# Kernel tuning notes

Measured on AMD Instinct MI355X. Metric: run time of the kernel, lower is better.

The kernel has to match this reference:

```python
import jax, jax.numpy as jnp
import numpy as np


def setup_inputs() -> dict:
    key = jax.random.key(0)
    kq, kk, kv, km = jax.random.split(key, 4)
    B, H, S, D = 2, 16, 2048, 64
    q = jax.random.normal(kq, (B, H, S, D), dtype=jnp.float32)
    k = jax.random.normal(kk, (B, H, S, D), dtype=jnp.float32)
    v = jax.random.normal(kv, (B, H, S, D), dtype=jnp.float32)
    mask = jax.random.randint(km, (B, 1, S, S), 0, 2, dtype=jnp.int32)
    return {"q": q, "k": k, "v": v, "mask": mask}


def reference(q, k, v, mask):
    # Scaled dot-product attention: softmax(Q K^T / sqrt(D)) V
    D = q.shape[-1]
    scale = jnp.asarray(1.0 / np.sqrt(D), q.dtype)
    score = jnp.einsum("bhqd,bhkd->bhqk", q, k) * scale  # [B,H,S,S]
    score = jnp.where(mask == 0, jnp.asarray(-10000.0, score.dtype), score)
    attn = jax.nn.softmax(score, axis=-1)
    out = jnp.einsum("bhqk,bhkd->bhqd", attn, v)  # [B,H,S,D]
    return (out, attn)
```

## Files before the change

### kernel.cpp

```cpp
#include <hip/hip_runtime.h>
#include <stdint.h>

typedef __attribute__((ext_vector_type(8))) short short8;
typedef __attribute__((ext_vector_type(4))) float f32x4;

#define B_ 2
#define H_ 16
#define S_ 2048
#define D_ 64
#define KB_ 64
#define NT_ (S_ / KB_)

__device__ __forceinline__ unsigned pk2(float x, float y) {
  const unsigned a = __builtin_bit_cast(unsigned, x) + 0x8000u;
  const unsigned b = __builtin_bit_cast(unsigned, y) + 0x8000u;
  return (a >> 16) | (b & 0xffff0000u);
}
__device__ __forceinline__ short b16(float x) {
  return (short)((__builtin_bit_cast(unsigned, x) + 0x8000u) >> 16);
}

__device__ __forceinline__ void block_barrier() {
  __asm__ volatile("s_waitcnt lgkmcnt(0)\n\ts_barrier" ::: "memory");
}
__device__ __forceinline__ void lgkm0() {
  __asm__ volatile("s_waitcnt lgkmcnt(0)" ::: "memory");
}

__global__ __launch_bounds__(256, 4)
void attn_kernel(const float* __restrict__ Q, const float* __restrict__ K,
                 const float* __restrict__ V, const int* __restrict__ M,
                 float* __restrict__ O, float* __restrict__ A)
{
  const int bid = blockIdx.x + (blockIdx.y << 5);
  const int qt  = (bid >> 3) & 31;
  const int bh  = (bid & 7) | ((bid >> 8) << 3);
  const int b   = bh >> 4;

  const int tid  = threadIdx.x;
  const int wave = tid >> 6;
  const int lane = tid & 63;
  const int l15  = lane & 15;
  const int quad = lane >> 4;

  const float* Qp = Q + (size_t)bh * S_ * D_;
  const float* Kp = K + (size_t)bh * S_ * D_;
  const float* Vp = V + (size_t)bh * S_ * D_;
  const int*   Mp = M + (size_t)b * S_ * S_;
  float* Op = O + (size_t)bh * S_ * D_;
  float* Ap = A + (size_t)bh * S_ * S_;

  const int q0 = qt * 64 + wave * 16;

  __shared__ __attribute__((aligned(16))) short Ks[64][72];
  __shared__ __attribute__((aligned(16))) short Vt[64][72];
  __shared__ __attribute__((aligned(16))) float Ps[4][16][68];

  short8 aq[2];
  {
    const float* qr = Qp + (size_t)(q0 + l15) * D_ + quad * 8;
#pragma unroll
    for (int h = 0; h < 2; ++h) {
      const float4 x0 = *(const float4*)(qr + h * 32);
      const float4 x1 = *(const float4*)(qr + h * 32 + 4);
      union { unsigned u[4]; short8 s; } u;
      u.u[0] = pk2(x0.x * 0.125f, x0.y * 0.125f);
      u.u[1] = pk2(x0.z * 0.125f, x0.w * 0.125f);
      u.u[2] = pk2(x1.x * 0.125f, x1.y * 0.125f);
      u.u[3] = pk2(x1.z * 0.125f, x1.w * 0.125f);
      aq[h] = u.s;
    }
  }

  const int srow = tid >> 2;
  const int scol = (tid & 3) * 4;
  const int lrow = lane >> 4;
  const int lcol = (lane & 15) * 4;

  float kbuf[16];
  float vbuf[16];

  auto loadK = [&](int kt) {
#pragma unroll
    for (int j = 0; j < 4; ++j) {
      const float4 x = *(const float4*)(Kp + (size_t)(kt + srow) * D_ + scol + 16 * j);
      kbuf[4*j+0] = x.x; kbuf[4*j+1] = x.y; kbuf[4*j+2] = x.z; kbuf[4*j+3] = x.w;
    }
  };
  auto writeK = [&]() {
#pragma unroll
    for (int j = 0; j < 4; ++j)
      *(uint2*)&Ks[srow][scol + 16*j] =
        make_uint2(pk2(kbuf[4*j+0], kbuf[4*j+1]), pk2(kbuf[4*j+2], kbuf[4*j+3]));
  };
  auto loadV = [&](int kt) {
#pragma unroll
    for (int u = 0; u < 4; ++u) {
      const float4 x = *(const float4*)(Vp + (size_t)(kt + srow) * D_ + scol + 16 * u);
      vbuf[4*u+0] = x.x; vbuf[4*u+1] = x.y; vbuf[4*u+2] = x.z; vbuf[4*u+3] = x.w;
    }
  };
  auto writeV = [&]() {
#pragma unroll
    for (int u = 0; u < 4; ++u) {
      const int kks = srow ^ (u << 4);
#pragma unroll
      for (int c = 0; c < 4; ++c)
        Vt[16*u + scol + c][kks] = b16(vbuf[4*u+c]);
    }
  };

  float lr[4];

  {
    float rowsum[4] = {0.f, 0.f, 0.f, 0.f};
    loadK(0);
    writeK();
    block_barrier();
    for (int t = 0; t < NT_; ++t) {
      const int kt = t * KB_;
      if (t + 1 < NT_) loadK(kt + KB_);
      int4 mr[4];
#pragma unroll
      for (int i = 0; i < 4; ++i)
        mr[i] = *(const int4*)(Mp + (size_t)(q0 + lrow + 4*i) * S_ + kt + lcol);

      f32x4 acc[4] = {{0,0,0,0},{0,0,0,0},{0,0,0,0},{0,0,0,0}};
      __builtin_amdgcn_s_setprio(1);
#pragma unroll
      for (int nt = 0; nt < 4; ++nt)
#pragma unroll
        for (int h = 0; h < 2; ++h) {
          const short8 bk = *(const short8*)&Ks[nt*16 + l15][h*32 + quad*8];
          acc[nt] = __builtin_amdgcn_mfma_f32_16x16x32_bf16(aq[h], bk, acc[nt], 0, 0, 0);
        }
      __builtin_amdgcn_s_setprio(0);
#pragma unroll
      for (int nt = 0; nt < 4; ++nt)
#pragma unroll
        for (int r = 0; r < 4; ++r)
          Ps[wave][quad*4 + r][nt*16 + l15] = acc[nt][r];
      lgkm0();
#pragma unroll
      for (int i = 0; i < 4; ++i) {
        const f32x4 s = *(const f32x4*)&Ps[wave][lrow + 4*i][lcol];
        const float e0 = mr[i].x ? __expf(s[0]) : 0.f;
        const float e1 = mr[i].y ? __expf(s[1]) : 0.f;
        const float e2 = mr[i].z ? __expf(s[2]) : 0.f;
        const float e3 = mr[i].w ? __expf(s[3]) : 0.f;
        rowsum[i] += (e0 + e1) + (e2 + e3);
      }
      block_barrier();
      if (t + 1 < NT_) writeK();
      block_barrier();
    }
#pragma unroll
    for (int i = 0; i < 4; ++i) {
      float s = rowsum[i];
      s += __shfl_xor(s, 1);
      s += __shfl_xor(s, 2);
      s += __shfl_xor(s, 4);
      s += __shfl_xor(s, 8);
      lr[i] = (s > 0.f) ? -__logf(s) : 0.f;
    }
  }

  f32x4 oacc[4] = {{0,0,0,0},{0,0,0,0},{0,0,0,0},{0,0,0,0}};
  loadK(0);
  loadV(0);
  writeK();
  writeV();
  block_barrier();
  for (int t = 0; t < NT_; ++t) {
    const int kt = t * KB_;
    if (t + 1 < NT_) { loadK(kt + KB_); loadV(kt + KB_); }
    int4 mr[4];
#pragma unroll
    for (int i = 0; i < 4; ++i)
      mr[i] = *(const int4*)(Mp + (size_t)(q0 + lrow + 4*i) * S_ + kt + lcol);

    f32x4 acc[4] = {{0,0,0,0},{0,0,0,0},{0,0,0,0},{0,0,0,0}};
    __builtin_amdgcn_s_setprio(1);
#pragma unroll
    for (int nt = 0; nt < 4; ++nt)
#pragma unroll
      for (int h = 0; h < 2; ++h) {
        const short8 bk = *(const short8*)&Ks[nt*16 + l15][h*32 + quad*8];
        acc[nt] = __builtin_amdgcn_mfma_f32_16x16x32_bf16(aq[h], bk, acc[nt], 0, 0, 0);
      }
    __builtin_amdgcn_s_setprio(0);
#pragma unroll
    for (int nt = 0; nt < 4; ++nt)
#pragma unroll
      for (int r = 0; r < 4; ++r)
        Ps[wave][quad*4 + r][nt*16 + l15] = acc[nt][r];
    lgkm0();

#pragma unroll
    for (int i = 0; i < 4; ++i) {
      const f32x4 s = *(const f32x4*)&Ps[wave][lrow + 4*i][lcol];
      const float lv = lr[i];
      f32x4 p;
      p[0] = __expf(mr[i].x ? s[0] + lv : -1e5f);
      p[1] = __expf(mr[i].y ? s[1] + lv : -1e5f);
      p[2] = __expf(mr[i].z ? s[2] + lv : -1e5f);
      p[3] = __expf(mr[i].w ? s[3] + lv : -1e5f);
      __builtin_nontemporal_store(p, (f32x4*)(Ap + (size_t)(q0 + lrow + 4*i) * S_ + kt + lcol));
      *(f32x4*)&Ps[wave][lrow + 4*i][lcol] = p;
    }
    lgkm0();

    short8 pa0, pa1;
    {
      const f32x4 q0v = *(const f32x4*)&Ps[wave][l15][quad*8];
      const f32x4 q1v = *(const f32x4*)&Ps[wave][l15][quad*8 + 4];
      const f32x4 q2v = *(const f32x4*)&Ps[wave][l15][32 + quad*8];
      const f32x4 q3v = *(const f32x4*)&Ps[wave][l15][32 + quad*8 + 4];
      union { unsigned u[4]; short8 s; } ua, ub;
      ua.u[0] = pk2(q0v[0], q0v[1]); ua.u[1] = pk2(q0v[2], q0v[3]);
      ua.u[2] = pk2(q1v[0], q1v[1]); ua.u[3] = pk2(q1v[2], q1v[3]);
      ub.u[0] = pk2(q2v[0], q2v[1]); ub.u[1] = pk2(q2v[2], q2v[3]);
      ub.u[2] = pk2(q3v[0], q3v[1]); ub.u[3] = pk2(q3v[2], q3v[3]);
      pa0 = ua.s; pa1 = ub.s;
    }
    __builtin_amdgcn_s_setprio(1);
#pragma unroll
    for (int nt = 0; nt < 4; ++nt) {
      const short8 bv0 = *(const short8*)&Vt[nt*16 + l15][(quad*8) ^ (nt << 4)];
      const short8 bv1 = *(const short8*)&Vt[nt*16 + l15][(32 + quad*8) ^ (nt << 4)];
      oacc[nt] = __builtin_amdgcn_mfma_f32_16x16x32_bf16(pa0, bv0, oacc[nt], 0, 0, 0);
      oacc[nt] = __builtin_amdgcn_mfma_f32_16x16x32_bf16(pa1, bv1, oacc[nt], 0, 0, 0);
    }
    __builtin_amdgcn_s_setprio(0);
    block_barrier();
    if (t + 1 < NT_) { writeK(); writeV(); }
    block_barrier();
  }

#pragma unroll
  for (int nt = 0; nt < 4; ++nt)
#pragma unroll
    for (int r = 0; r < 4; ++r)
      Op[(size_t)(q0 + quad*4 + r) * D_ + nt*16 + l15] = oacc[nt][r];
}

extern "C" void kernel_launch(void* const* d_in, const int* in_sizes, int n_in,
                              void* d_out, int out_size, void* d_ws, size_t ws_size,
                              hipStream_t stream) {
  const float* q = (const float*)d_in[0];
  const float* k = (const float*)d_in[1];
  const float* v = (const float*)d_in[2];
  const int*   m = (const int*)d_in[3];
  float* out  = (float*)d_out;
  float* attn = out + (size_t)B_ * H_ * S_ * D_;

  dim3 grid(S_ / 64, B_ * H_);
  attn_kernel<<<grid, 256, 0, stream>>>(q, k, v, m, out, attn);
}
```

Before: 736.9 us.

## Compute softmax directly in MFMA layout, cache mask bits, stage P as bf16

Removes the fp32 LDS round-trip of scores by applying the mask, exp and sum directly on MFMA accumulator registers. The mask is read once in the first pass and kept as per-lane bitmasks, so the second pass no longer reloads it from global memory. P is written to LDS as bf16 in the layout the PV MFMA reads, and the V transpose is rewritten to use packed 8-byte LDS stores. Scaling is folded into log2e so exp2f/log2f replace expf/logf. The risks are attention stores and mask loads that become scalar 4-byte accesses with a 16-lane stride, and more register pressure from mreg.

```diff
diff --git a/kernel.cpp b/kernel.cpp
--- a/kernel.cpp
+++ b/kernel.cpp
@@ -46,69 +46,72 @@
   const float* Qp = Q + (size_t)bh * S_ * D_;
   const float* Kp = K + (size_t)bh * S_ * D_;
   const float* Vp = V + (size_t)bh * S_ * D_;
-  const int*   Mp = M + (size_t)b * S_ * S_;
   float* Op = O + (size_t)bh * S_ * D_;
-  float* Ap = A + (size_t)bh * S_ * S_;
 
   const int q0 = qt * 64 + wave * 16;
+
+  const int*  Mrow = M + (size_t)b  * S_ * S_ + (size_t)(q0 + 4 * quad) * S_ + l15;
+  float*      Arow = A + (size_t)bh * S_ * S_ + (size_t)(q0 + 4 * quad) * S_ + l15;
 
   __shared__ __attribute__((aligned(16))) short Ks[64][72];
   __shared__ __attribute__((aligned(16))) short Vt[64][72];
-  __shared__ __attribute__((aligned(16))) float Ps[4][16][68];
+  __shared__ __attribute__((aligned(16))) short Pb[4][16][72];
 
   short8 aq[2];
   {
+    const float c = 0.18033688011112042f;
     const float* qr = Qp + (size_t)(q0 + l15) * D_ + quad * 8;
 #pragma unroll
     for (int h = 0; h < 2; ++h) {
       const float4 x0 = *(const float4*)(qr + h * 32);
       const float4 x1 = *(const float4*)(qr + h * 32 + 4);
       union { unsigned u[4]; short8 s; } u;
-      u.u[0] = pk2(x0.x * 0.125f, x0.y * 0.125f);
-      u.u[1] = pk2(x0.z * 0.125f, x0.w * 0.125f);
-      u.u[2] = pk2(x1.x * 0.125f, x1.y * 0.125f);
-      u.u[3] = pk2(x1.z * 0.125f, x1.w * 0.125f);
+      u.u[0] = pk2(x0.x * c, x0.y * c);
+      u.u[1] = pk2(x0.z * c, x0.w * c);
+      u.u[2] = pk2(x1.x * c, x1.y * c);
+      u.u[3] = pk2(x1.z * c, x1.w * c);
       aq[h] = u.s;
     }
   }
 
-  const int srow = tid >> 2;
-  const int scol = (tid & 3) * 4;
-  const int lrow = lane >> 4;
-  const int lcol = (lane & 15) * 4;
+  const int ksr = tid >> 2;
+  const int ksc = (tid & 3) * 4;
+  const int vr4 = (tid & 15) * 4;
+  const int vdc = (tid >> 4) * 4;
 
   float kbuf[16];
-  float vbuf[16];
+  float vbuf[4][4];
 
   auto loadK = [&](int kt) {
 #pragma unroll
     for (int j = 0; j < 4; ++j) {
-      const float4 x = *(const float4*)(Kp + (size_t)(kt + srow) * D_ + scol + 16 * j);
+      const float4 x = *(const float4*)(Kp + (size_t)(kt + ksr) * D_ + ksc + 16 * j);
       kbuf[4*j+0] = x.x; kbuf[4*j+1] = x.y; kbuf[4*j+2] = x.z; kbuf[4*j+3] = x.w;
     }
   };
   auto writeK = [&]() {
 #pragma unroll
     for (int j = 0; j < 4; ++j)
-      *(uint2*)&Ks[srow][scol + 16*j] =
+      *(uint2*)&Ks[ksr][ksc + 16*j] =
         make_uint2(pk2(kbuf[4*j+0], kbuf[4*j+1]), pk2(kbuf[4*j+2], kbuf[4*j+3]));
   };
   auto loadV = [&](int kt) {
 #pragma unroll
-    for (int u = 0; u < 4; ++u) {
-      const float4 x = *(const float4*)(Vp + (size_t)(kt + srow) * D_ + scol + 16 * u);
-      vbuf[4*u+0] = x.x; vbuf[4*u+1] = x.y; vbuf[4*u+2] = x.z; vbuf[4*u+3] = x.w;
+    for (int i = 0; i < 4; ++i) {
+      const float4 x = *(const float4*)(Vp + (size_t)(kt + vr4 + i) * D_ + vdc);
+      vbuf[i][0] = x.x; vbuf[i][1] = x.y; vbuf[i][2] = x.z; vbuf[i][3] = x.w;
     }
   };
   auto writeV = [&]() {
 #pragma unroll
-    for (int u = 0; u < 4; ++u) {
-      const int kks = srow ^ (u << 4);
-#pragma unroll
-      for (int c = 0; c < 4; ++c)
-        Vt[16*u + scol + c][kks] = b16(vbuf[4*u+c]);
-    }
-  };
+    for (int c = 0; c < 4; ++c)
+      *(uint2*)&Vt[vdc + c][vr4] =
+        make_uint2(pk2(vbuf[0][c], vbuf[1][c]), pk2(vbuf[2][c], vbuf[3][c]));
+  };
+
+  unsigned mreg[16];
+#pragma unroll
+  for (int i = 0; i < 16; ++i) mreg[i] = 0u;
 
   float lr[4];
 
@@ -120,10 +123,12 @@
     for (int t = 0; t < NT_; ++t) {
       const int kt = t * KB_;
       if (t + 1 < NT_) loadK(kt + KB_);
-      int4 mr[4];
-#pragma unroll
-      for (int i = 0; i < 4; ++i)
-        mr[i] = *(const int4*)(Mp + (size_t)(q0 + lrow + 4*i) * S_ + kt + lcol);
+      int mv[16];
+#pragma unroll
+      for (int nt = 0; nt < 4; ++nt)
+#pragma unroll
+        for (int r = 0; r < 4; ++r)
+          mv[nt*4+r] = Mrow[(size_t)r * S_ + kt + 16*nt];
 
       f32x4 acc[4] = {{0,0,0,0},{0,0,0,0},{0,0,0,0},{0,0,0,0}};
       __builtin_amdgcn_s_setprio(1);
@@ -138,18 +143,11 @@
 #pragma unroll
       for (int nt = 0; nt < 4; ++nt)
 #pragma unroll
-        for (int r = 0; r < 4; ++r)
-          Ps[wave][quad*4 + r][nt*16 + l15] = acc[nt][r];
-      lgkm0();
-#pragma unroll
-      for (int i = 0; i < 4; ++i) {
-        const f32x4 s = *(const f32x4*)&Ps[wave][lrow + 4*i][lcol];
-        const float e0 = mr[i].x ? __expf(s[0]) : 0.f;
-        const float e1 = mr[i].y ? __expf(s[1]) : 0.f;
-        const float e2 = mr[i].z ? __expf(s[2]) : 0.f;
-        const float e3 = mr[i].w ? __expf(s[3]) : 0.f;
-        rowsum[i] += (e0 + e1) + (e2 + e3);
-      }
+        for (int r = 0; r < 4; ++r) {
+          const unsigned p = (mv[nt*4+r] != 0) ? 1u : 0u;
+          mreg[nt*4+r] |= p << t;
+          rowsum[r] += p ? exp2f(acc[nt][r]) : 0.f;
+        }
       block_barrier();
       if (t + 1 < NT_) writeK();
       block_barrier();
@@ -161,7 +159,7 @@
       s += __shfl_xor(s, 2);
       s += __shfl_xor(s, 4);
       s += __shfl_xor(s, 8);
-      lr[i] = (s > 0.f) ? -__logf(s) : 0.f;
+      lr[i] = (s > 0.f) ? -__log2f(s) : 0.f;
     }
   }
 
@@ -174,10 +172,6 @@
   for (int t = 0; t < NT_; ++t) {
     const int kt = t * KB_;
     if (t + 1 < NT_) { loadK(kt + KB_); loadV(kt + KB_); }
-    int4 mr[4];
-#pragma unroll
-    for (int i = 0; i < 4; ++i)
-      mr[i] = *(const int4*)(Mp + (size_t)(q0 + lrow + 4*i) * S_ + kt + lcol);
 
     f32x4 acc[4] = {{0,0,0,0},{0,0,0,0},{0,0,0,0},{0,0,0,0}};
     __builtin_amdgcn_s_setprio(1);
@@ -189,45 +183,26 @@
         acc[nt] = __builtin_amdgcn_mfma_f32_16x16x32_bf16(aq[h], bk, acc[nt], 0, 0, 0);
       }
     __builtin_amdgcn_s_setprio(0);
+
 #pragma unroll
     for (int nt = 0; nt < 4; ++nt)
 #pragma unroll
-      for (int r = 0; r < 4; ++r)
-        Ps[wave][quad*4 + r][nt*16 + l15] = acc[nt][r];
+      for (int r = 0; r < 4; ++r) {
+        const unsigned bit = (mreg[nt*4+r] >> t) & 1u;
+        const float sarg = bit ? (acc[nt][r] + lr[r]) : -1.0e5f;
+        const float p = exp2f(sarg);
+        __builtin_nontemporal_store(p, Arow + (size_t)r * S_ + kt + 16*nt);
+        Pb[wave][quad*4 + r][nt*16 + l15] = b16(p);
+      }
     lgkm0();
 
-#pragma unroll
-    for (int i = 0; i < 4; ++i) {
-      const f32x4 s = *(const f32x4*)&Ps[wave][lrow + 4*i][lcol];
-      const float lv = lr[i];
-      f32x4 p;
-      p[0] = __expf(mr[i].x ? s[0] + lv : -1e5f);
-      p[1] = __expf(mr[i].y ? s[1] + lv : -1e5f);
-      p[2] = __expf(mr[i].z ? s[2] + lv : -1e5f);
-      p[3] = __expf(mr[i].w ? s[3] + lv : -1e5f);
-      __builtin_nontemporal_store(p, (f32x4*)(Ap + (size_t)(q0 + lrow + 4*i) * S_ + kt + lcol));
-      *(f32x4*)&Ps[wave][lrow + 4*i][lcol] = p;
-    }
-    lgkm0();
-
-    short8 pa0, pa1;
-    {
-      const f32x4 q0v = *(const f32x4*)&Ps[wave][l15][quad*8];
-      const f32x4 q1v = *(const f32x4*)&Ps[wave][l15][quad*8 + 4];
-      const f32x4 q2v = *(const f32x4*)&Ps[wave][l15][32 + quad*8];
-      const f32x4 q3v = *(const f32x4*)&Ps[wave][l15][32 + quad*8 + 4];
-      union { unsigned u[4]; short8 s; } ua, ub;
-      ua.u[0] = pk2(q0v[0], q0v[1]); ua.u[1] = pk2(q0v[2], q0v[3]);
-      ua.u[2] = pk2(q1v[0], q1v[1]); ua.u[3] = pk2(q1v[2], q1v[3]);
-      ub.u[0] = pk2(q2v[0], q2v[1]); ub.u[1] = pk2(q2v[2], q2v[3]);
-      ub.u[2] = pk2(q3v[0], q3v[1]); ub.u[3] = pk2(q3v[2], q3v[3]);
-      pa0 = ua.s; pa1 = ub.s;
-    }
+    const short8 pa0 = *(const short8*)&Pb[wave][l15][quad*8];
+    const short8 pa1 = *(const short8*)&Pb[wave][l15][32 + quad*8];
     __builtin_amdgcn_s_setprio(1);
 #pragma unroll
     for (int nt = 0; nt < 4; ++nt) {
-      const short8 bv0 = *(const short8*)&Vt[nt*16 + l15][(quad*8) ^ (nt << 4)];
-      const short8 bv1 = *(const short8*)&Vt[nt*16 + l15][(32 + quad*8) ^ (nt << 4)];
+      const short8 bv0 = *(const short8*)&Vt[nt*16 + l15][quad*8];
+      const short8 bv1 = *(const short8*)&Vt[nt*16 + l15][32 + quad*8];
       oacc[nt] = __builtin_amdgcn_mfma_f32_16x16x32_bf16(pa0, bv0, oacc[nt], 0, 0, 0);
       oacc[nt] = __builtin_amdgcn_mfma_f32_16x16x32_bf16(pa1, bv1, oacc[nt], 0, 0, 0);
     }
```

Measured after the change: 767.4 us. 4.1% more time.
